# Kernel optimization log

Hardware: AMD Instinct MI355X
Metric: run time of the kernel (lower is better)

The kernel has to match this reference:

```python
import jax, jax.numpy as jnp
import numpy as np

N, D, P = 100000, 4, 300  # hits, condensation-space dim, number of true particles
Q_MIN = 0.01
RADIUS_THRESHOLD = 10.0
PT_THLD = 0.9


def setup_inputs() -> dict:
    key = jax.random.key(0)
    kb, kx, kr, kt = jax.random.split(key, 4)
    beta = jax.random.uniform(kb, (N,), jnp.float32, 1e-3, 0.9)  # in (0,1) for arctanh
    x = jax.random.normal(kx, (N, D), dtype=jnp.float32)
    # every pid in 1..P appears; pid 0 is noise -> torch.unique(pid[pid>0]) == arange(1, P+1)
    particle_id = (jnp.arange(N, dtype=jnp.int32) % (P + 1)).astype(jnp.int32)
    reconstructable = jax.random.randint(kr, (N,), 0, 2, dtype=jnp.int32)
    track_params = jax.random.uniform(kt, (N,), jnp.float32, 0.0, 2.0)  # pt [GeV]
    return {
        "beta": beta,
        "x": x,
        "particle_id": particle_id,
        "reconstructable": reconstructable,
        "track_params": track_params,
    }


def reference(beta, x, particle_id, reconstructable, track_params):
    pids = jnp.arange(1, P + 1, dtype=particle_id.dtype)  # == unique(pid[pid>0]) by construction
    mask = (reconstructable > 0) & (track_params > PT_THLD)  # [N] bool

    pid_masks = particle_id[:, None] == pids[None, :]  # [N, P] bool
    q = jnp.arctanh(beta) ** 2 + Q_MIN  # [N]

    # condensation centers: per-pid argmax of charge q
    alphas = jnp.argmax(q[:, None] * pid_masks, axis=0)  # [P]
    x_a = x[alphas]  # [P, D]
    q_a = q[alphas]  # [P]

    diff = x[:, None, :] - x_a[None, :, :]  # [N, P, D]
    norm_sq = jnp.sum(diff * diff, axis=-1)  # [N, P]

    va = q[:, None] * pid_masks * (norm_sq * q_a[None, :])  # attractive potential
    vr = (
        q[:, None]
        * (~pid_masks)
        * (jax.nn.relu(RADIUS_THRESHOLD - jnp.sqrt(norm_sq + 1e-8)) * q_a[None, :])
    )  # repulsive potential

    maskf = mask.astype(va.dtype)
    # torch.mean(va[mask], dim=0) == masked column mean
    attractive = jnp.sum(jnp.sum(va * maskf[:, None], axis=0) / jnp.sum(maskf))
    repulsive = jnp.sum(jnp.mean(vr, axis=0))
    return jnp.stack([attractive, repulsive])
```

## Files before the change

### kernel.cpp

```cpp
#include <hip/hip_runtime.h>
#include <math.h>

#define N_HITS 100000
#define P_PART 300
#define NSPLIT 20
#define PB (P_PART / NSPLIT)
#define HPT 4
#define TILE (256 * HPT)
#define NBINS 512
#define KA_BLOCKS 80
#define Q_MIN 0.01f
#define R_THLD 10.0f
#define PT_THLD 0.9f


__global__ __launch_bounds__(256) void kA_scan(
        const float* __restrict__ beta,
        const float* __restrict__ x,
        const int* __restrict__ pid,
        const int* __restrict__ recon,
        const float* __restrict__ tp,
        unsigned long long* __restrict__ best,
        unsigned int* __restrict__ nmask,
        unsigned int* __restrict__ doneA,
        float4* __restrict__ c) {
    __shared__ unsigned long long bloc[P_PART];
    __shared__ int sCnt[4];
    __shared__ int isLast;
    for (int s = threadIdx.x; s < P_PART; s += 256) bloc[s] = 0ULL;
    __syncthreads();

    int cnt = 0;
    for (int i = blockIdx.x * 256 + threadIdx.x; i < N_HITS; i += KA_BLOCKS * 256) {
        int p = pid[i];
        if (p > 0) {
            unsigned long long pack =
                ((unsigned long long)__float_as_uint(beta[i]) << 32) |
                (unsigned long long)(~(unsigned int)i);
            atomicMax(&bloc[p - 1], pack);
        }
        cnt += (recon[i] > 0 && tp[i] > PT_THLD) ? 1 : 0;
    }
    __syncthreads();

    for (int s = threadIdx.x; s < P_PART; s += 256) {
        unsigned long long v = bloc[s];
        if (v) atomicMax(&best[s], v);
    }
    #pragma unroll
    for (int off = 32; off > 0; off >>= 1) cnt += __shfl_down(cnt, off, 64);
    if ((threadIdx.x & 63) == 0) sCnt[threadIdx.x >> 6] = cnt;
    __threadfence();
    __syncthreads();
    if (threadIdx.x == 0) {
        atomicAdd(nmask, (unsigned int)(sCnt[0] + sCnt[1] + sCnt[2] + sCnt[3]));
        unsigned int old = atomicAdd(doneA, 1u);
        isLast = (old == (unsigned int)(KA_BLOCKS - 1)) ? 1 : 0;
    }
    __syncthreads();
    if (isLast) {
        for (int s = threadIdx.x; s < P_PART; s += 256) {
            unsigned long long b = atomicOr(&best[s], 0ULL);
            unsigned int idx = (b == 0ULL) ? 0u : ~(unsigned int)(b & 0xffffffffULL);
            float a = atanhf(beta[idx]);
            float4 xa = reinterpret_cast<const float4*>(x)[idx];
            float na = xa.x * xa.x + xa.y * xa.y + xa.z * xa.z + xa.w * xa.w;
            c[2 * s] = xa;
            c[2 * s + 1] = make_float4(na, a * a + Q_MIN, 0.f, 0.f);
        }
    }
}

__global__ __launch_bounds__(256, 8) void kB_main(
        const float* __restrict__ beta,
        const float* __restrict__ x,
        const int* __restrict__ pid,
        const int* __restrict__ recon,
        const float* __restrict__ tp,
        const float4* __restrict__ c,
        double* __restrict__ bins) {
    __shared__ float4 xa_s[PB];
    __shared__ float2 nq_s[PB];
    int p0 = blockIdx.y * PB;
    if (threadIdx.x < PB) {
        float4 r1 = c[2 * (p0 + threadIdx.x) + 1];
        xa_s[threadIdx.x] = c[2 * (p0 + threadIdx.x)];
        nq_s[threadIdx.x] = make_float2(r1.x, r1.y);
    }
    __syncthreads();

    int base = blockIdx.x * TILE + threadIdx.x;
    float4 m2[HPT];
    float  sx[HPT];
    float  q[HPT], aq[HPT], racc[HPT];
    int    pm1[HPT];
    #pragma unroll
    for (int h = 0; h < HPT; ++h) {
        int i = base + h * 256;
        bool valid = (i < N_HITS);
        int ii = valid ? i : 0;
        float4 xi = reinterpret_cast<const float4*>(x)[ii];
        m2[h] = make_float4(-2.f * xi.x, -2.f * xi.y, -2.f * xi.z, -2.f * xi.w);
        sx[h] = xi.x * xi.x + xi.y * xi.y + xi.z * xi.z + xi.w * xi.w + 1e-8f;
        float a = atanhf(beta[ii]);
        q[h] = valid ? (a * a + Q_MIN) : 0.f;
        pm1[h] = valid ? (pid[ii] - 1) : -1;
        aq[h] = (valid && recon[ii] > 0 && tp[ii] > PT_THLD) ? q[h] : 0.f;
        racc[h] = 0.f;
    }

    #pragma unroll 5
    for (int p = 0; p < PB; ++p) {
        float4 xa = xa_s[p];
        float2 nq = nq_s[p];
        #pragma unroll
        for (int h = 0; h < HPT; ++h) {
            float n = sx[h] + nq.x;
            n = fmaf(m2[h].x, xa.x, n);
            n = fmaf(m2[h].y, xa.y, n);
            n = fmaf(m2[h].z, xa.z, n);
            n = fmaf(m2[h].w, xa.w, n);
            float s = __builtin_amdgcn_sqrtf(fmaxf(n, 0.f));
            racc[h] = fmaf(fmaxf(R_THLD - s, 0.f), nq.y, racc[h]);
        }
    }

    float att = 0.f, rep = 0.f;
    #pragma unroll
    for (int h = 0; h < HPT; ++h) {
        int lp = pm1[h] - p0;
        if (lp >= 0 && lp < PB) {
            float4 xa = xa_s[lp];
            float2 nq = nq_s[lp];
            float n = sx[h] + nq.x;
            n = fmaf(m2[h].x, xa.x, n);
            n = fmaf(m2[h].y, xa.y, n);
            n = fmaf(m2[h].z, xa.z, n);
            n = fmaf(m2[h].w, xa.w, n);
            float s = __builtin_amdgcn_sqrtf(fmaxf(n, 0.f));
            racc[h] -= fmaxf(R_THLD - s, 0.f) * nq.y;
            att += aq[h] * (n - 1e-8f) * nq.y;
        }
        rep += q[h] * racc[h];
    }

    #pragma unroll
    for (int off = 32; off > 0; off >>= 1) {
        att += __shfl_down(att, off, 64);
        rep += __shfl_down(rep, off, 64);
    }
    __shared__ float sA[4], sR[4];
    int wid = threadIdx.x >> 6;
    if ((threadIdx.x & 63) == 0) { sA[wid] = att; sR[wid] = rep; }
    __syncthreads();
    if (threadIdx.x == 0) {
        float A = sA[0] + sA[1] + sA[2] + sA[3];
        float R = sR[0] + sR[1] + sR[2] + sR[3];
        int bin = (int)((blockIdx.y * gridDim.x + blockIdx.x) & (NBINS - 1));
        atomicAdd(&bins[2 * bin], (double)A);
        atomicAdd(&bins[2 * bin + 1], (double)R);
    }
}

__global__ __launch_bounds__(256) void kC_fin(
        const double* __restrict__ bins,
        const unsigned int* __restrict__ nmask,
        float* __restrict__ out) {
    double a = 0.0, r = 0.0;
    for (int t = threadIdx.x; t < NBINS; t += 256) {
        a += bins[2 * t];
        r += bins[2 * t + 1];
    }
    #pragma unroll
    for (int off = 32; off > 0; off >>= 1) {
        a += __shfl_down(a, off, 64);
        r += __shfl_down(r, off, 64);
    }
    __shared__ double dA[4], dR[4];
    int wid = threadIdx.x >> 6;
    if ((threadIdx.x & 63) == 0) { dA[wid] = a; dR[wid] = r; }
    __syncthreads();
    if (threadIdx.x == 0) {
        a = dA[0] + dA[1] + dA[2] + dA[3];
        r = dR[0] + dR[1] + dR[2] + dR[3];
        out[0] = (float)(a / (double)(*nmask));
        out[1] = (float)(r / (double)N_HITS);
    }
}

extern "C" void kernel_launch(void* const* d_in, const int* in_sizes, int n_in,
                              void* d_out, int out_size, void* d_ws, size_t ws_size,
                              hipStream_t stream) {
    const float* beta  = (const float*)d_in[0];
    const float* x     = (const float*)d_in[1];
    const int*   pid   = (const int*)d_in[2];
    const int*   recon = (const int*)d_in[3];
    const float* tp    = (const float*)d_in[4];
    float* out = (float*)d_out;

    char* ws = (char*)d_ws;
    unsigned long long* best  = (unsigned long long*)(ws);
    unsigned int*       doneA = (unsigned int*)(ws + 2400);
    unsigned int*       nmask = (unsigned int*)(ws + 2408);
    double*             bins  = (double*)(ws + 2432);
    float4*             c     = (float4*)(ws + 10624);

    const int nblocksBx = (N_HITS + TILE - 1) / TILE;

    hipMemsetAsync(d_ws, 0, 10624, stream);

    kA_scan<<<KA_BLOCKS, 256, 0, stream>>>(beta, x, pid, recon, tp,
                                           best, nmask, doneA, c);
    kB_main<<<dim3(nblocksBx, NSPLIT), 256, 0, stream>>>(beta, x, pid, recon, tp,
                                                         c, bins);
    kC_fin<<<1, 256, 0, stream>>>(bins, nmask, out);
}
```

Before: 97.06 us.

## Precompute charge with sign-encoded mask, partition argmax by pid range, drop memset

The first kernel now computes q = atanh(beta)^2 + qmin once per hit and stores it with the sign bit carrying the reconstructable/pt mask. That removes the per-split atanh and the recon/tp loads from the main kernel, which previously repeated them across 20 splits. Each first-kernel block owns 3 pids and scans all pid values with shared-memory atomics, which replaces the global atomics and the last-block election. It also zeroes the bins in place of hipMemsetAsync and writes per-block mask counts. The main kernel doubles hits per thread and lowers occupancy bounds. Risks: each block now scans the full pid array redundantly (100 blocks × 400KB), and zeroing bins inside kA only works because kB runs after it on the same stream.

Result: slower. 143.3 us (+47.6%).

```diff
diff --git a/kernel.cpp b/kernel.cpp
--- a/kernel.cpp
+++ b/kernel.cpp
@@ -2,81 +2,110 @@
 #include <math.h>
 
 #define N_HITS 100000
+#define NH4 (N_HITS / 4)
 #define P_PART 300
+#define KA_BLOCKS 100
+#define PPB 3
 #define NSPLIT 20
 #define PB (P_PART / NSPLIT)
-#define HPT 4
+#define HPT 8
 #define TILE (256 * HPT)
+#define NBX ((N_HITS + TILE - 1) / TILE)
 #define NBINS 512
-#define KA_BLOCKS 80
 #define Q_MIN 0.01f
 #define R_THLD 10.0f
 #define PT_THLD 0.9f
 
 
-__global__ __launch_bounds__(256) void kA_scan(
+__global__ __launch_bounds__(256) void kA_prep(
         const float* __restrict__ beta,
         const float* __restrict__ x,
         const int* __restrict__ pid,
         const int* __restrict__ recon,
         const float* __restrict__ tp,
-        unsigned long long* __restrict__ best,
-        unsigned int* __restrict__ nmask,
-        unsigned int* __restrict__ doneA,
-        float4* __restrict__ c) {
-    __shared__ unsigned long long bloc[P_PART];
+        float4* __restrict__ c,
+        float4* __restrict__ q4,
+        unsigned int* __restrict__ cntb,
+        unsigned long long* __restrict__ wsZero) {
+    __shared__ unsigned long long bloc[PPB];
     __shared__ int sCnt[4];
-    __shared__ int isLast;
-    for (int s = threadIdx.x; s < P_PART; s += 256) bloc[s] = 0ULL;
-    __syncthreads();
-
+    int tid = threadIdx.x, bid = blockIdx.x;
+    if (tid < PPB) bloc[tid] = 0ULL;
+    {
+        int g = bid * 256 + tid;
+        if (g < 1024) wsZero[g] = 0ULL;
+    }
+
+    const float4* b4 = (const float4*)beta;
+    const int4*   r4 = (const int4*)recon;
+    const float4* t4 = (const float4*)tp;
     int cnt = 0;
-    for (int i = blockIdx.x * 256 + threadIdx.x; i < N_HITS; i += KA_BLOCKS * 256) {
-        int p = pid[i];
-        if (p > 0) {
-            unsigned long long pack =
-                ((unsigned long long)__float_as_uint(beta[i]) << 32) |
-                (unsigned long long)(~(unsigned int)i);
-            atomicMax(&bloc[p - 1], pack);
-        }
-        cnt += (recon[i] > 0 && tp[i] > PT_THLD) ? 1 : 0;
-    }
-    __syncthreads();
-
-    for (int s = threadIdx.x; s < P_PART; s += 256) {
-        unsigned long long v = bloc[s];
-        if (v) atomicMax(&best[s], v);
+    if (tid < 250) {
+        int j = bid * 250 + tid;
+        float4 b = b4[j];
+        int4   rc = r4[j];
+        float4 t = t4[j];
+        float4 qo;
+        {
+            float a = atanhf(b.x); float qv = a * a + Q_MIN;
+            bool mk = (rc.x > 0) && (t.x > PT_THLD); cnt += mk; qo.x = mk ? -qv : qv;
+        }
+        {
+            float a = atanhf(b.y); float qv = a * a + Q_MIN;
+            bool mk = (rc.y > 0) && (t.y > PT_THLD); cnt += mk; qo.y = mk ? -qv : qv;
+        }
+        {
+            float a = atanhf(b.z); float qv = a * a + Q_MIN;
+            bool mk = (rc.z > 0) && (t.z > PT_THLD); cnt += mk; qo.z = mk ? -qv : qv;
+        }
+        {
+            float a = atanhf(b.w); float qv = a * a + Q_MIN;
+            bool mk = (rc.w > 0) && (t.w > PT_THLD); cnt += mk; qo.w = mk ? -qv : qv;
+        }
+        q4[j] = qo;
     }
     #pragma unroll
     for (int off = 32; off > 0; off >>= 1) cnt += __shfl_down(cnt, off, 64);
-    if ((threadIdx.x & 63) == 0) sCnt[threadIdx.x >> 6] = cnt;
-    __threadfence();
-    __syncthreads();
-    if (threadIdx.x == 0) {
-        atomicAdd(nmask, (unsigned int)(sCnt[0] + sCnt[1] + sCnt[2] + sCnt[3]));
-        unsigned int old = atomicAdd(doneA, 1u);
-        isLast = (old == (unsigned int)(KA_BLOCKS - 1)) ? 1 : 0;
-    }
-    __syncthreads();
-    if (isLast) {
-        for (int s = threadIdx.x; s < P_PART; s += 256) {
-            unsigned long long b = atomicOr(&best[s], 0ULL);
-            unsigned int idx = (b == 0ULL) ? 0u : ~(unsigned int)(b & 0xffffffffULL);
-            float a = atanhf(beta[idx]);
-            float4 xa = reinterpret_cast<const float4*>(x)[idx];
-            float na = xa.x * xa.x + xa.y * xa.y + xa.z * xa.z + xa.w * xa.w;
-            c[2 * s] = xa;
-            c[2 * s + 1] = make_float4(na, a * a + Q_MIN, 0.f, 0.f);
-        }
-    }
-}
-
-__global__ __launch_bounds__(256, 8) void kB_main(
-        const float* __restrict__ beta,
+    if ((tid & 63) == 0) sCnt[tid >> 6] = cnt;
+    __syncthreads();
+    if (tid == 0) cntb[bid] = (unsigned)(sCnt[0] + sCnt[1] + sCnt[2] + sCnt[3]);
+
+    int lo = 1 + PPB * bid;
+    const int4* p4 = (const int4*)pid;
+    for (int j = tid; j < NH4; j += 256) {
+        int4 pv = p4[j];
+        int base = 4 * j;
+        #pragma unroll
+        for (int e = 0; e < 4; ++e) {
+            int p = (&pv.x)[e];
+            unsigned u = (unsigned)(p - lo);
+            if (u < PPB) {
+                int i = base + e;
+                unsigned long long pack =
+                    ((unsigned long long)__float_as_uint(beta[i]) << 32) |
+                    (unsigned long long)(~(unsigned)i);
+                atomicMax(&bloc[u], pack);
+            }
+        }
+    }
+    __syncthreads();
+
+    if (tid < PPB) {
+        unsigned long long b = bloc[tid];
+        unsigned idx = (b == 0ULL) ? 0u : ~(unsigned)(b & 0xffffffffULL);
+        float a = atanhf(beta[idx]);
+        float4 xa = ((const float4*)x)[idx];
+        float na = xa.x * xa.x + xa.y * xa.y + xa.z * xa.z + xa.w * xa.w;
+        int pd = PPB * bid + tid;
+        c[2 * pd] = xa;
+        c[2 * pd + 1] = make_float4(na, a * a + Q_MIN, 0.f, 0.f);
+    }
+}
+
+__global__ __launch_bounds__(256, 4) void kB_main(
         const float* __restrict__ x,
         const int* __restrict__ pid,
-        const int* __restrict__ recon,
-        const float* __restrict__ tp,
+        const float* __restrict__ q_arr,
         const float4* __restrict__ c,
         double* __restrict__ bins) {
     __shared__ float4 xa_s[PB];
@@ -99,17 +128,18 @@
         int i = base + h * 256;
         bool valid = (i < N_HITS);
         int ii = valid ? i : 0;
-        float4 xi = reinterpret_cast<const float4*>(x)[ii];
+        float4 xi = ((const float4*)x)[ii];
         m2[h] = make_float4(-2.f * xi.x, -2.f * xi.y, -2.f * xi.z, -2.f * xi.w);
         sx[h] = xi.x * xi.x + xi.y * xi.y + xi.z * xi.z + xi.w * xi.w + 1e-8f;
-        float a = atanhf(beta[ii]);
-        q[h] = valid ? (a * a + Q_MIN) : 0.f;
+        float qraw = q_arr[ii];
+        float qv = fabsf(qraw);
+        q[h]  = valid ? qv : 0.f;
+        aq[h] = (valid && qraw < 0.f) ? qv : 0.f;
         pm1[h] = valid ? (pid[ii] - 1) : -1;
-        aq[h] = (valid && recon[ii] > 0 && tp[ii] > PT_THLD) ? q[h] : 0.f;
         racc[h] = 0.f;
     }
 
-    #pragma unroll 5
+    #pragma unroll 3
     for (int p = 0; p < PB; ++p) {
         float4 xa = xa_s[p];
         float2 nq = nq_s[p];
@@ -164,26 +194,31 @@
 
 __global__ __launch_bounds__(256) void kC_fin(
         const double* __restrict__ bins,
-        const unsigned int* __restrict__ nmask,
+        const unsigned int* __restrict__ cntb,
         float* __restrict__ out) {
     double a = 0.0, r = 0.0;
+    long long cnt = 0;
     for (int t = threadIdx.x; t < NBINS; t += 256) {
         a += bins[2 * t];
         r += bins[2 * t + 1];
     }
+    if (threadIdx.x < KA_BLOCKS) cnt = (long long)cntb[threadIdx.x];
     #pragma unroll
     for (int off = 32; off > 0; off >>= 1) {
         a += __shfl_down(a, off, 64);
         r += __shfl_down(r, off, 64);
+        cnt += __shfl_down(cnt, off, 64);
     }
     __shared__ double dA[4], dR[4];
+    __shared__ long long dC[4];
     int wid = threadIdx.x >> 6;
-    if ((threadIdx.x & 63) == 0) { dA[wid] = a; dR[wid] = r; }
+    if ((threadIdx.x & 63) == 0) { dA[wid] = a; dR[wid] = r; dC[wid] = cnt; }
     __syncthreads();
     if (threadIdx.x == 0) {
         a = dA[0] + dA[1] + dA[2] + dA[3];
         r = dR[0] + dR[1] + dR[2] + dR[3];
-        out[0] = (float)(a / (double)(*nmask));
+        cnt = dC[0] + dC[1] + dC[2] + dC[3];
+        out[0] = (float)(a / (double)cnt);
         out[1] = (float)(r / (double)N_HITS);
     }
 }
@@ -199,19 +234,15 @@
     float* out = (float*)d_out;
 
     char* ws = (char*)d_ws;
-    unsigned long long* best  = (unsigned long long*)(ws);
-    unsigned int*       doneA = (unsigned int*)(ws + 2400);
-    unsigned int*       nmask = (unsigned int*)(ws + 2408);
-    double*             bins  = (double*)(ws + 2432);
-    float4*             c     = (float4*)(ws + 10624);
-
-    const int nblocksBx = (N_HITS + TILE - 1) / TILE;
-
-    hipMemsetAsync(d_ws, 0, 10624, stream);
-
-    kA_scan<<<KA_BLOCKS, 256, 0, stream>>>(beta, x, pid, recon, tp,
-                                           best, nmask, doneA, c);
-    kB_main<<<dim3(nblocksBx, NSPLIT), 256, 0, stream>>>(beta, x, pid, recon, tp,
-                                                         c, bins);
-    kC_fin<<<1, 256, 0, stream>>>(bins, nmask, out);
-}
+    double*             bins  = (double*)(ws);
+    unsigned int*       cntb  = (unsigned int*)(ws + 8192);
+    float4*             c     = (float4*)(ws + 8704);
+    float4*             q4    = (float4*)(ws + 18304);
+    float*              q_arr = (float*)(ws + 18304);
+    unsigned long long* wsZ   = (unsigned long long*)(ws);
+
+    kA_prep<<<KA_BLOCKS, 256, 0, stream>>>(beta, x, pid, recon, tp,
+                                           c, q4, cntb, wsZ);
+    kB_main<<<dim3(NBX, NSPLIT), 256, 0, stream>>>(x, pid, q_arr, c, bins);
+    kC_fin<<<1, 256, 0, stream>>>(bins, cntb, out);
+}
```
